# Kernel tuning notes

Hardware: AMD Instinct MI355X
Metric: run time of the kernel (lower is better)

Reference implementation:

```python
import jax, jax.numpy as jnp
import numpy as np

N_HEADS = 16

def setup_inputs() -> dict:
    key = jax.random.key(0)
    ks = jax.random.split(key, 6)
    B, T, C = 8, 1024, 1024
    x = jax.random.normal(ks[0], (B, T, C), dtype=jnp.float32)
    s = 0.02
    Wk = jax.random.normal(ks[1], (C, C), dtype=jnp.float32) * s
    Wq = jax.random.normal(ks[2], (C, C), dtype=jnp.float32) * s
    Wv = jax.random.normal(ks[3], (C, C), dtype=jnp.float32) * s
    Wp = jax.random.normal(ks[4], (C, C), dtype=jnp.float32) * s
    bp = jax.random.normal(ks[5], (C,), dtype=jnp.float32) * s
    return {"x": x, "Wk": Wk, "Wq": Wq, "Wv": Wv, "Wp": Wp, "bp": bp}


def reference(x, Wk, Wq, Wv, Wp, bp):
    B, T, C = x.shape
    D = C // N_HEADS
    # torch Linear: y = x @ W^T
    def heads(W):
        h = (x @ W.T).reshape(B, T, N_HEADS, D)
        return jnp.transpose(h, (0, 2, 1, 3))  # [B,H,T,D]
    k, q, v = heads(Wk), heads(Wq), heads(Wv)
    # NOTE: source computes k @ q^T (rows index keys, cols index queries)
    att = jnp.einsum('bhid,bhjd->bhij', k, q) * (D ** -0.5)
    mask = jnp.tril(jnp.ones((T, T), dtype=bool))  # masked_fill where mask==0
    att = jnp.where(mask, att, -jnp.inf)
    att = jax.nn.softmax(att, axis=-1)
    y = jnp.einsum('bhij,bhjd->bhid', att, v)  # [B,H,T,D]
    y = jnp.transpose(y, (0, 2, 1, 3)).reshape(B, T, C)
    return y @ Wp.T + bp
```

## Files before the change

### kernel.cpp

```cpp
#include <hip/hip_runtime.h>
#include <hip/hip_bf16.h>


typedef __attribute__((ext_vector_type(8))) short short8;
typedef __attribute__((ext_vector_type(8))) unsigned short ushort8;
typedef __attribute__((ext_vector_type(4))) unsigned short ushort4_t;
typedef __attribute__((ext_vector_type(4))) unsigned int uintx4;
typedef __attribute__((ext_vector_type(4))) float floatx4;

#define LOG2E 1.44269504088896f

__device__ __forceinline__ unsigned short f2bf(float f) {
  unsigned int u = __float_as_uint(f);
  u += 0x7FFFu + ((u >> 16) & 1u);
  return (unsigned short)(u >> 16);
}

__device__ __forceinline__ unsigned int pack2bf(float lo, float hi) {
  return (unsigned int)f2bf(lo) | ((unsigned int)f2bf(hi) << 16);
}

__device__ __forceinline__ void gload_lds16(const void* g, void* l) {
  __builtin_amdgcn_global_load_lds(
      (const __attribute__((address_space(1))) unsigned int*)g,
      (__attribute__((address_space(3))) unsigned int*)l, 16, 0, 0);
}

__global__ __launch_bounds__(256) void cast_all_kernel(
    const float* __restrict__ x, const float* __restrict__ Wk,
    const float* __restrict__ Wq, const float* __restrict__ Wv,
    const float* __restrict__ Wp, unsigned short* __restrict__ xb,
    unsigned short* __restrict__ wb) {
  int idx = blockIdx.x * 256 + threadIdx.x;
  for (int i = idx; i < 1572864; i += 2048 * 256) {
    const float* src;
    unsigned short* dst;
    if (i < 1048576) {
      src = x + (size_t)i * 8;
      dst = xb + (size_t)i * 8;
    } else {
      int j = i - 1048576;
      int sel = j >> 17;
      int o = (j & 131071) * 8;
      const float* wsrc = sel == 0 ? Wk : sel == 1 ? Wq : sel == 2 ? Wv : Wp;
      src = wsrc + o;
      dst = wb + (size_t)sel * 1048576 + o;
    }
    const float4* p = reinterpret_cast<const float4*>(src);
    float4 a = p[0], b = p[1];
    ushort8 r;
    r[0] = f2bf(a.x); r[1] = f2bf(a.y); r[2] = f2bf(a.z); r[3] = f2bf(a.w);
    r[4] = f2bf(b.x); r[5] = f2bf(b.y); r[6] = f2bf(b.z); r[7] = f2bf(b.w);
    *reinterpret_cast<ushort8*>(dst) = r;
  }
}

template <int MODE, int NB>
__global__ __launch_bounds__(256) void gemm2_kernel(
    const unsigned short* __restrict__ A, const unsigned short* __restrict__ Bb,
    unsigned short* __restrict__ outb, float* __restrict__ outf,
    const float* __restrict__ bias) {
  const int tid = threadIdx.x;
  const int lane = tid & 63;
  const int w = tid >> 6;
  const int wr = w >> 1, wc = w & 1;
  const int g = lane >> 4, r = lane & 15;

  constexpr int NWG = NB * 64;
  constexpr int CPX = NWG / 8;
  const int bid = blockIdx.x;
  const int wgid = (bid & 7) * CPX + (bid >> 3);
  const int mb = wgid / NB, nb = wgid % NB;
  const int m0 = mb * 128, n0 = nb * 128;

  __shared__ unsigned short sA[2][128 * 64];
  __shared__ unsigned short sB[2][128 * 64];

  floatx4 acc[4][4];
#pragma unroll
  for (int i = 0; i < 4; ++i)
#pragma unroll
    for (int j = 0; j < 4; ++j) acc[i][j] = (floatx4)0.0f;

  const int su = lane >> 3;
  const int sc = (lane & 7) ^ su;

  auto stage = [&](int bsel, int kt) {
#pragma unroll
    for (int u = 0; u < 4; ++u) {
      const int row = u * 32 + w * 8 + su;
      gload_lds16(&A[(size_t)(m0 + row) * 1024 + kt * 64 + sc * 8],
                  &sA[bsel][(u * 32 + w * 8) * 64]);
      gload_lds16(&Bb[(size_t)(n0 + row) * 1024 + kt * 64 + sc * 8],
                  &sB[bsel][(u * 32 + w * 8) * 64]);
    }
  };

  int buf = 0;
  stage(0, 0);
  __syncthreads();

  for (int kt = 0; kt < 16; ++kt) {
    if (kt < 15) stage(buf ^ 1, kt + 1);
#pragma unroll
    for (int kk = 0; kk < 2; ++kk) {
      short8 aF[4], bF[4];
#pragma unroll
      for (int mf = 0; mf < 4; ++mf) {
        const int row = wr * 64 + mf * 16 + r;
        aF[mf] = *reinterpret_cast<const short8*>(
            &sA[buf][row * 64 + (((kk * 4 + g) ^ (r & 7)) * 8)]);
      }
#pragma unroll
      for (int nf = 0; nf < 4; ++nf) {
        const int row = wc * 64 + nf * 16 + r;
        bF[nf] = *reinterpret_cast<const short8*>(
            &sB[buf][row * 64 + (((kk * 4 + g) ^ (r & 7)) * 8)]);
      }
#pragma unroll
      for (int mf = 0; mf < 4; ++mf)
#pragma unroll
        for (int nf = 0; nf < 4; ++nf)
          acc[mf][nf] = __builtin_amdgcn_mfma_f32_16x16x32_bf16(
              aF[mf], bF[nf], acc[mf][nf], 0, 0, 0);
    }
    __syncthreads();
    buf ^= 1;
  }

  if (MODE == 0) {
    const int zB = n0 >> 10;
    unsigned short* outz = outb + (size_t)zB * 8388608;
    if (zB == 2) {
#pragma unroll
      for (int mf = 0; mf < 4; ++mf)
#pragma unroll
        for (int nf = 0; nf < 4; ++nf) {
          int m = m0 + wr * 64 + mf * 16 + g * 4;
          int nn = n0 + wc * 64 + nf * 16 + r;
          int b = m >> 10, t = m & 1023, h = (nn & 1023) >> 6, d = nn & 63;
          ushort4_t pk;
          pk[0] = f2bf(acc[mf][nf][0]); pk[1] = f2bf(acc[mf][nf][1]);
          pk[2] = f2bf(acc[mf][nf][2]); pk[3] = f2bf(acc[mf][nf][3]);
          *reinterpret_cast<ushort4_t*>(
              &outz[((size_t)((b * 16 + h) * 64 + d)) * 1024 + t]) = pk;
        }
    } else {
#pragma unroll
      for (int mf = 0; mf < 4; ++mf)
#pragma unroll
        for (int nf = 0; nf < 4; ++nf)
#pragma unroll
          for (int q = 0; q < 4; ++q) {
            int m = m0 + wr * 64 + mf * 16 + g * 4 + q;
            int nn = n0 + wc * 64 + nf * 16 + r;
            int b = m >> 10, t = m & 1023, h = (nn & 1023) >> 6, d = nn & 63;
            outz[(size_t)((b * 16 + h) * 1024 + t) * 64 + d] = f2bf(acc[mf][nf][q]);
          }
    }
  } else {
#pragma unroll
    for (int mf = 0; mf < 4; ++mf)
#pragma unroll
      for (int nf = 0; nf < 4; ++nf) {
        int nn = n0 + wc * 64 + nf * 16 + r;
        float bv = bias[nn];
#pragma unroll
        for (int q = 0; q < 4; ++q) {
          int m = m0 + wr * 64 + mf * 16 + g * 4 + q;
          outf[(size_t)m * 1024 + nn] = acc[mf][nf][q] + bv;
        }
      }
  }
}

__device__ __forceinline__ void softmax_pv_tile(
    floatx4 (&sT)[4], const unsigned short* __restrict__ Vb,
    floatx4 (&accYT)[4], float& m_run, float& l_run,
    int g, int r, int j0, int i_lane, bool diag) {
#pragma unroll
  for (int jf = 0; jf < 4; ++jf)
#pragma unroll
    for (int q = 0; q < 4; ++q) {
      float v = sT[jf][q] * 0.125f;
      if (diag && (j0 + jf * 16 + g * 4 + q > i_lane)) v = -1e30f;
      sT[jf][q] = v;
    }
  float mx = sT[0][0];
#pragma unroll
  for (int jf = 0; jf < 4; ++jf)
#pragma unroll
    for (int q = 0; q < 4; ++q) mx = fmaxf(mx, sT[jf][q]);
  mx = fmaxf(mx, __shfl_xor(mx, 16));
  mx = fmaxf(mx, __shfl_xor(mx, 32));
  float mnew = fmaxf(m_run, mx);
  float corr = exp2f((m_run - mnew) * LOG2E);
  m_run = mnew;
  float ssum = 0.0f;
#pragma unroll
  for (int jf = 0; jf < 4; ++jf)
#pragma unroll
    for (int q = 0; q < 4; ++q) {
      float p = exp2f((sT[jf][q] - mnew) * LOG2E);
      sT[jf][q] = p;
      ssum += p;
    }
  ssum += __shfl_xor(ssum, 16);
  ssum += __shfl_xor(ssum, 32);
  l_run = l_run * corr + ssum;
#pragma unroll
  for (int df = 0; df < 4; ++df) accYT[df] *= corr;
  unsigned int pk[4][2];
#pragma unroll
  for (int jf = 0; jf < 4; ++jf) {
    pk[jf][0] = pack2bf(sT[jf][0], sT[jf][1]);
    pk[jf][1] = pack2bf(sT[jf][2], sT[jf][3]);
  }
  short8 bP[2];
#pragma unroll
  for (int s = 0; s < 2; ++s) {
    uintx4 wd;
#pragma unroll
    for (int w_ = 0; w_ < 4; ++w_) {
      int src = (((g & 1) * 2 + (w_ >> 1)) << 4) + r;
      unsigned int t0 = (unsigned int)__shfl((int)pk[2 * s][w_ & 1], src);
      unsigned int t1 = (unsigned int)__shfl((int)pk[2 * s + 1][w_ & 1], src);
      wd[w_] = (g & 2) ? t1 : t0;
    }
    bP[s] = __builtin_bit_cast(short8, wd);
  }
  __builtin_amdgcn_s_setprio(1);
#pragma unroll
  for (int df = 0; df < 4; ++df) {
#pragma unroll
    for (int s = 0; s < 2; ++s) {
      short8 av = *reinterpret_cast<const short8*>(
          &Vb[(df * 16 + r) * 64 + ((s * 32 + g * 8) ^ ((r & 7) * 8))]);
      accYT[df] = __builtin_amdgcn_mfma_f32_16x16x32_bf16(av, bP[s], accYT[df], 0, 0, 0);
    }
  }
  __builtin_amdgcn_s_setprio(0);
}

__global__ __launch_bounds__(256, 4) void attn_kernel(
    const unsigned short* __restrict__ kqv, unsigned short* __restrict__ y) {
  const int tid = threadIdx.x;
  const int lane = tid & 63;
  const int w = tid >> 6;
  const int g = lane >> 4, r = lane & 15;
  const int bh = blockIdx.y;
  const int z = blockIdx.x;
  const int itA = z, itB = 15 - z;
  const int iwA = itA * 64 + w * 16;
  const int iwB = itB * 64 + w * 16;

  const unsigned short* Kh = kqv + (size_t)bh * 65536;
  const unsigned short* Qh = kqv + 8388608u + (size_t)bh * 65536;
  const unsigned short* Vt = kqv + 16777216u + (size_t)bh * 65536;

  __shared__ unsigned short Qs[2][64 * 64];
  __shared__ unsigned short Vs[2][64 * 64];

  short8 bKA[2], bKB[2];
#pragma unroll
  for (int s = 0; s < 2; ++s) {
    bKA[s] = *reinterpret_cast<const short8*>(&Kh[(size_t)(iwA + r) * 64 + s * 32 + g * 8]);
    bKB[s] = *reinterpret_cast<const short8*>(&Kh[(size_t)(iwB + r) * 64 + s * 32 + g * 8]);
  }

  floatx4 accA[4], accB[4];
#pragma unroll
  for (int df = 0; df < 4; ++df) { accA[df] = (floatx4)0.0f; accB[df] = (floatx4)0.0f; }
  float mA = -1e30f, lA = 0.0f, mB = -1e30f, lB = 0.0f;

  auto stage = [&](int bsel, int jts) {
    const int j0s = jts * 64;
    const int c = lane & 7;
#pragma unroll
    for (int u = 0; u < 2; ++u) {
      const int R = w * 16 + u * 8 + (lane >> 3);
      const int cc = c ^ (R & 7);
      gload_lds16(&Qh[(size_t)(j0s + R) * 64 + cc * 8], &Qs[bsel][(w * 16 + u * 8) * 64]);
      gload_lds16(&Vt[(size_t)R * 1024 + j0s + cc * 8], &Vs[bsel][(w * 16 + u * 8) * 64]);
    }
  };

  int buf = 0;
  stage(0, 0);
  __syncthreads();

  for (int jt = 0; jt <= itB; ++jt) {
    const int j0 = jt * 64;
    if (jt < itB) stage(buf ^ 1, jt + 1);

    const unsigned short* Qb = &Qs[buf][0];
    const unsigned short* Vb = &Vs[buf][0];

    floatx4 sT[4];
    __builtin_amdgcn_s_setprio(1);
#pragma unroll
    for (int jf = 0; jf < 4; ++jf) {
      sT[jf] = (floatx4)0.0f;
#pragma unroll
      for (int s = 0; s < 2; ++s) {
        short8 aq = *reinterpret_cast<const short8*>(
            &Qb[(jf * 16 + r) * 64 + ((s * 32 + g * 8) ^ ((r & 7) * 8))]);
        sT[jf] = __builtin_amdgcn_mfma_f32_16x16x32_bf16(aq, bKB[s], sT[jf], 0, 0, 0);
      }
    }
    __builtin_amdgcn_s_setprio(0);
    softmax_pv_tile(sT, Vb, accB, mB, lB, g, r, j0, iwB + r, jt == itB);

    if (jt <= itA) {
      floatx4 sA2[4];
      __builtin_amdgcn_s_setprio(1);
#pragma unroll
      for (int jf = 0; jf < 4; ++jf) {
        sA2[jf] = (floatx4)0.0f;
#pragma unroll
        for (int s = 0; s < 2; ++s) {
          short8 aq = *reinterpret_cast<const short8*>(
              &Qb[(jf * 16 + r) * 64 + ((s * 32 + g * 8) ^ ((r & 7) * 8))]);
          sA2[jf] = __builtin_amdgcn_mfma_f32_16x16x32_bf16(aq, bKA[s], sA2[jf], 0, 0, 0);
        }
      }
      __builtin_amdgcn_s_setprio(0);
      softmax_pv_tile(sA2, Vb, accA, mA, lA, g, r, j0, iwA + r, jt == itA);
    }

    __syncthreads();
    buf ^= 1;
  }

  const int b = bh >> 4, h = bh & 15;
#pragma unroll
  for (int tile = 0; tile < 2; ++tile) {
    const floatx4* acc = tile ? accB : accA;
    const float inv = 1.0f / (tile ? lB : lA);
    const int t = (tile ? iwB : iwA) + r;
    unsigned short* row = y + (size_t)(b * 1024 + t) * 1024 + h * 64;
#pragma unroll
    for (int df = 0; df < 4; ++df) {
      ushort4_t pkv;
      pkv[0] = f2bf(acc[df][0] * inv);
      pkv[1] = f2bf(acc[df][1] * inv);
      pkv[2] = f2bf(acc[df][2] * inv);
      pkv[3] = f2bf(acc[df][3] * inv);
      *reinterpret_cast<ushort4_t*>(&row[df * 16 + g * 4]) = pkv;
    }
  }
}

extern "C" void kernel_launch(void* const* d_in, const int* in_sizes, int n_in,
                              void* d_out, int out_size, void* d_ws, size_t ws_size,
                              hipStream_t stream) {
  const float* x  = (const float*)d_in[0];
  const float* Wk = (const float*)d_in[1];
  const float* Wq = (const float*)d_in[2];
  const float* Wv = (const float*)d_in[3];
  const float* Wp = (const float*)d_in[4];
  const float* bp = (const float*)d_in[5];
  float* out = (float*)d_out;

  char* ws = (char*)d_ws;
  unsigned short* xb  = (unsigned short*)ws;
  unsigned short* wb  = (unsigned short*)(ws + (16u << 20));
  unsigned short* kqv = (unsigned short*)(ws + (24u << 20));

  cast_all_kernel<<<2048, 256, 0, stream>>>(x, Wk, Wq, Wv, Wp, xb, wb);

  gemm2_kernel<0, 24><<<1536, 256, 0, stream>>>(xb, wb, kqv, nullptr, nullptr);

  attn_kernel<<<dim3(8, 128), 256, 0, stream>>>(kqv, xb );

  gemm2_kernel<1, 8><<<512, 256, 0, stream>>>(xb, wb + 3 * 1048576, nullptr, out, bp);
}
```

Measured before the change: 246.0 us.

## Triple-buffer GEMM K-tiles with 32-wide stages and explicit vmcnt waits

Rewrites the GEMM main loop from double buffering of 64-wide K tiles to triple buffering of 32-wide K tiles. Global-to-LDS loads run two stages ahead, and explicit s_waitcnt vmcnt counts plus sched_barrier replace the full __syncthreads drain. Global addresses are precomputed per thread and the LDS swizzle is adapted to 4 chunks. The aim is to hide load latency better, at the cost of twice as many barriers per K and smaller MFMA batches per stage.

```diff
diff --git a/kernel.cpp b/kernel.cpp
--- a/kernel.cpp
+++ b/kernel.cpp
@@ -56,7 +56,7 @@
 }
 
 template <int MODE, int NB>
-__global__ __launch_bounds__(256) void gemm2_kernel(
+__global__ __launch_bounds__(256) void gemm3_kernel(
     const unsigned short* __restrict__ A, const unsigned short* __restrict__ Bb,
     unsigned short* __restrict__ outb, float* __restrict__ outf,
     const float* __restrict__ bias) {
@@ -73,8 +73,8 @@
   const int mb = wgid / NB, nb = wgid % NB;
   const int m0 = mb * 128, n0 = nb * 128;
 
-  __shared__ unsigned short sA[2][128 * 64];
-  __shared__ unsigned short sB[2][128 * 64];
+  __shared__ unsigned short sA[3][128 * 32];
+  __shared__ unsigned short sB[3][128 * 32];
 
   floatx4 acc[4][4];
 #pragma unroll
@@ -82,50 +82,63 @@
 #pragma unroll
     for (int j = 0; j < 4; ++j) acc[i][j] = (floatx4)0.0f;
 
-  const int su = lane >> 3;
-  const int sc = (lane & 7) ^ su;
+  const int srow = w * 16 + (lane >> 2);
+  const int sc = (lane & 3) ^ ((lane >> 2) & 3);
+  const char* gA0 = (const char*)(A + (size_t)(m0 + srow) * 1024) + sc * 16;
+  const char* gA1 = (const char*)(A + (size_t)(m0 + 64 + srow) * 1024) + sc * 16;
+  const char* gB0 = (const char*)(Bb + (size_t)(n0 + srow) * 1024) + sc * 16;
+  const char* gB1 = (const char*)(Bb + (size_t)(n0 + 64 + srow) * 1024) + sc * 16;
 
   auto stage = [&](int bsel, int kt) {
-#pragma unroll
-    for (int u = 0; u < 4; ++u) {
-      const int row = u * 32 + w * 8 + su;
-      gload_lds16(&A[(size_t)(m0 + row) * 1024 + kt * 64 + sc * 8],
-                  &sA[bsel][(u * 32 + w * 8) * 64]);
-      gload_lds16(&Bb[(size_t)(n0 + row) * 1024 + kt * 64 + sc * 8],
-                  &sB[bsel][(u * 32 + w * 8) * 64]);
-    }
+    const size_t off = (size_t)kt * 64;
+    gload_lds16(gA0 + off, &sA[bsel][(w * 16) * 32]);
+    gload_lds16(gA1 + off, &sA[bsel][(64 + w * 16) * 32]);
+    gload_lds16(gB0 + off, &sB[bsel][(w * 16) * 32]);
+    gload_lds16(gB1 + off, &sB[bsel][(64 + w * 16) * 32]);
   };
 
-  int buf = 0;
   stage(0, 0);
-  __syncthreads();
-
-  for (int kt = 0; kt < 16; ++kt) {
-    if (kt < 15) stage(buf ^ 1, kt + 1);
-#pragma unroll
-    for (int kk = 0; kk < 2; ++kk) {
-      short8 aF[4], bF[4];
-#pragma unroll
-      for (int mf = 0; mf < 4; ++mf) {
-        const int row = wr * 64 + mf * 16 + r;
-        aF[mf] = *reinterpret_cast<const short8*>(
-            &sA[buf][row * 64 + (((kk * 4 + g) ^ (r & 7)) * 8)]);
-      }
-#pragma unroll
-      for (int nf = 0; nf < 4; ++nf) {
-        const int row = wc * 64 + nf * 16 + r;
-        bF[nf] = *reinterpret_cast<const short8*>(
-            &sB[buf][row * 64 + (((kk * 4 + g) ^ (r & 7)) * 8)]);
-      }
-#pragma unroll
-      for (int mf = 0; mf < 4; ++mf)
-#pragma unroll
-        for (int nf = 0; nf < 4; ++nf)
-          acc[mf][nf] = __builtin_amdgcn_mfma_f32_16x16x32_bf16(
-              aF[mf], bF[nf], acc[mf][nf], 0, 0, 0);
-    }
-    __syncthreads();
-    buf ^= 1;
+  stage(1, 1);
+  asm volatile("s_waitcnt vmcnt(4)" ::: "memory");
+  __builtin_amdgcn_sched_barrier(0);
+  __builtin_amdgcn_s_barrier();
+
+  int bcur = 0;
+  for (int kt = 0; kt < 32; ++kt) {
+    if (kt < 30) {
+      stage(bcur == 0 ? 2 : bcur - 1, kt + 2);
+      asm volatile("s_waitcnt vmcnt(8)" ::: "memory");
+    } else if (kt == 30) {
+      asm volatile("s_waitcnt vmcnt(4)" ::: "memory");
+    } else {
+      asm volatile("s_waitcnt vmcnt(0)" ::: "memory");
+    }
+    __builtin_amdgcn_sched_barrier(0);
+
+    short8 aF[4], bF[4];
+#pragma unroll
+    for (int mf = 0; mf < 4; ++mf) {
+      const int row = wr * 64 + mf * 16 + r;
+      aF[mf] = *reinterpret_cast<const short8*>(
+          &sA[bcur][row * 32 + ((g ^ (r & 3)) * 8)]);
+    }
+#pragma unroll
+    for (int nf = 0; nf < 4; ++nf) {
+      const int row = wc * 64 + nf * 16 + r;
+      bF[nf] = *reinterpret_cast<const short8*>(
+          &sB[bcur][row * 32 + ((g ^ (r & 3)) * 8)]);
+    }
+#pragma unroll
+    for (int mf = 0; mf < 4; ++mf)
+#pragma unroll
+      for (int nf = 0; nf < 4; ++nf)
+        acc[mf][nf] = __builtin_amdgcn_mfma_f32_16x16x32_bf16(
+            aF[mf], bF[nf], acc[mf][nf], 0, 0, 0);
+
+    asm volatile("s_waitcnt lgkmcnt(0)" ::: "memory");
+    __builtin_amdgcn_sched_barrier(0);
+    __builtin_amdgcn_s_barrier();
+    bcur = (bcur == 2) ? 0 : bcur + 1;
   }
 
   if (MODE == 0) {
@@ -369,9 +382,9 @@
 
   cast_all_kernel<<<2048, 256, 0, stream>>>(x, Wk, Wq, Wv, Wp, xb, wb);
 
-  gemm2_kernel<0, 24><<<1536, 256, 0, stream>>>(xb, wb, kqv, nullptr, nullptr);
+  gemm3_kernel<0, 24><<<1536, 256, 0, stream>>>(xb, wb, kqv, nullptr, nullptr);
 
   attn_kernel<<<dim3(8, 128), 256, 0, stream>>>(kqv, xb );
 
-  gemm2_kernel<1, 8><<<512, 256, 0, stream>>>(xb, wb + 3 * 1048576, nullptr, out, bp);
-}
+  gemm3_kernel<1, 8><<<512, 256, 0, stream>>>(xb, wb + 3 * 1048576, nullptr, out, bp);
+}
```

Result: slower. 263.6 us (+7.1%).
